# Optimization experiments

Hardware: AMD Instinct MI355X
Metric: run time of the kernel (lower is better)

Reference implementation:

```python
import jax, jax.numpy as jnp
import numpy as np

B, L, D, H, DK = 4, 256, 512, 8, 64
NEG_INF = 1.0e9


def setup_inputs() -> dict:
    key = jax.random.key(0)
    ks = jax.random.split(key, 12)
    s = 1.0 / np.sqrt(D)
    inp = {
        "q": jax.random.normal(ks[0], (B, L, D), jnp.float32),
        "k": jax.random.normal(ks[1], (B, L, D), jnp.float32),
        "v": jax.random.normal(ks[2], (B, L, D), jnp.float32),
        "mask": jnp.ones((B, L, L), jnp.int32),
        "Wq": jax.random.normal(ks[3], (D, D), jnp.float32) * s,
        "bq": jnp.zeros((D,), jnp.float32),
        "Wk": jax.random.normal(ks[4], (D, D), jnp.float32) * s,
        "bk": jnp.zeros((D,), jnp.float32),
        "Wv": jax.random.normal(ks[5], (D, D), jnp.float32) * s,
        "bv": jnp.zeros((D,), jnp.float32),
        "vp": jax.random.normal(ks[6], (1, H, 1, 1, DK), jnp.float32) * 0.1,
        "W0": jax.random.normal(ks[7], (D, D), jnp.float32) * s,
        "b0": jnp.zeros((D,), jnp.float32),
    }
    return inp


def reference(q, k, v, mask, Wq, bq, Wk, bk, Wv, bv, vp, W0, b0):
    # project and split heads: (B, L, D) -> (B, H, L, DK)
    qh = (q @ Wq + bq).reshape(B, L, H, DK).transpose(0, 2, 1, 3)
    kh = (k @ Wk + bk).reshape(B, L, H, DK).transpose(0, 2, 1, 3)
    vh = (v @ Wv + bv).reshape(B, L, H, DK).transpose(0, 2, 1, 3)
    # additive (Bahdanau) scoring: (B, H, Lq, Lk, DK) intermediate
    energy = jnp.tanh(qh[:, :, :, None, :] + kh[:, :, None, :, :])
    scores = jnp.sum(vp * energy, axis=-1)  # (B, H, Lq, Lk)
    scores = jnp.where(mask[:, None] == 0, -NEG_INF, scores)
    attn = jax.nn.softmax(scores, axis=-1)
    out = jnp.matmul(attn, vh)  # (B, H, Lq, DK)
    out = out.transpose(0, 2, 1, 3).reshape(B, L, D)
    return out @ W0 + b0
```

## Files before the change

### kernel.cpp

```cpp
#include <hip/hip_runtime.h>

#define LSEQ 256
#define DMODEL 512
#define NHEAD 8
#define DKH 64
#define BATCH 4

#define TWO_LOG2E 2.885390081777927f

using short8 = __attribute__((ext_vector_type(8))) short;
using f32x4  = __attribute__((ext_vector_type(4))) float;

__device__ __forceinline__ void split4(const float* f, ushort4& h, ushort4& l) {
  unsigned short hh[4], ll[4];
#pragma unroll
  for (int j = 0; j < 4; ++j) {
    unsigned int u = __float_as_uint(f[j]);
    hh[j] = (unsigned short)(u >> 16);
    float hf = __uint_as_float(u & 0xFFFF0000u);
    ll[j] = (unsigned short)(__float_as_uint(f[j] - hf) >> 16);
  }
  h = make_ushort4(hh[0], hh[1], hh[2], hh[3]);
  l = make_ushort4(ll[0], ll[1], ll[2], ll[3]);
}

__device__ __forceinline__ void split8(float4 f0, float4 f1, short8& h, short8& l) {
  float f[8] = {f0.x, f0.y, f0.z, f0.w, f1.x, f1.y, f1.z, f1.w};
#pragma unroll
  for (int j = 0; j < 8; ++j) {
    unsigned int u = __float_as_uint(f[j]);
    h[j] = (short)(u >> 16);
    float hf = __uint_as_float(u & 0xFFFF0000u);
    l[j] = (short)(__float_as_uint(f[j] - hf) >> 16);
  }
}

__global__ __launch_bounds__(256) void prep_w_kernel(
    const float* __restrict__ Wq, const float* __restrict__ Wk,
    const float* __restrict__ Wv, const float* __restrict__ W0,
    unsigned short* __restrict__ whi, unsigned short* __restrict__ wlo)
{
  const int tid = threadIdx.x;
  const int g = blockIdx.z;
  const float* W = (g == 0) ? Wq : (g == 1) ? Wk : (g == 2) ? Wv : W0;
  const float scale = (g < 2) ? TWO_LOG2E : 1.0f;
  const int k0 = blockIdx.x * 32, n0 = blockIdx.y * 32;
  __shared__ float tile[32][36];
  {
    const int r = tid >> 3, c = (tid & 7) << 2;
    float4 f = *(const float4*)&W[(k0 + r) * DMODEL + n0 + c];
    tile[r][c + 0] = f.x * scale;
    tile[r][c + 1] = f.y * scale;
    tile[r][c + 2] = f.z * scale;
    tile[r][c + 3] = f.w * scale;
  }
  __syncthreads();
  const int n = tid >> 3, kk = (tid & 7) << 2;
  float x[4];
#pragma unroll
  for (int j = 0; j < 4; ++j) x[j] = tile[kk + j][n];
  ushort4 h4, l4;
  split4(x, h4, l4);
  const int base = (g * DMODEL + n0 + n) * DMODEL + k0 + kk;
  *(ushort4*)&whi[base] = h4;
  *(ushort4*)&wlo[base] = l4;
}

__device__ __forceinline__ void gemm_fp32A(
    const float* __restrict__ X,
    const unsigned short* __restrict__ wh, const unsigned short* __restrict__ wl,
    const float* __restrict__ bias, float bscale,
    float* __restrict__ out, int mode, int bx, int by)
{
  __shared__ short8 lds[2][4][512];
  const int tid = threadIdx.x;
  const int lane = tid & 63, w = tid >> 6;
  const int bm0 = bx * 64, bn0 = by * 64;

  const int r0 = tid >> 3, c0 = tid & 7, g0 = c0 ^ (r0 & 7);
  const int r1 = r0 + 32,  g1 = c0 ^ (r1 & 7);
  const size_t aoff0 = (size_t)(bm0 + r0) * DMODEL + g0 * 8;
  const size_t aoff1 = (size_t)(bm0 + r1) * DMODEL + g1 * 8;
  const size_t boff0 = (size_t)(bn0 + r0) * DMODEL + g0 * 8;
  const size_t boff1 = (size_t)(bn0 + r1) * DMODEL + g1 * 8;

  const int mrb = (w >> 1) << 5, ncb = (w & 1) << 5;
  const int l15 = lane & 15, lh = lane >> 4, l7 = lane & 7;

  float4 af00, af01, af10, af11;
  short8 b0h, b0l, b1h, b1l;

#define LOADS(K)                                                  \
  { af00 = *(const float4*)(X + aoff0 + (K));                     \
    af01 = *(const float4*)(X + aoff0 + (K) + 4);                 \
    af10 = *(const float4*)(X + aoff1 + (K));                     \
    af11 = *(const float4*)(X + aoff1 + (K) + 4);                 \
    b0h = *(const short8*)(wh + boff0 + (K));                     \
    b0l = *(const short8*)(wl + boff0 + (K));                     \
    b1h = *(const short8*)(wh + boff1 + (K));                     \
    b1l = *(const short8*)(wl + boff1 + (K)); }
#define WRITES(BUF)                                               \
  { short8 h_, l_;                                                \
    split8(af00, af01, h_, l_);                                   \
    lds[BUF][0][tid] = h_; lds[BUF][1][tid] = l_;                 \
    split8(af10, af11, h_, l_);                                   \
    lds[BUF][0][tid + 256] = h_; lds[BUF][1][tid + 256] = l_;     \
    lds[BUF][2][tid] = b0h; lds[BUF][3][tid] = b0l;               \
    lds[BUF][2][tid + 256] = b1h; lds[BUF][3][tid + 256] = b1l; }

  f32x4 acc[2][2] = {};
  LOADS(0);
  WRITES(0);
  __syncthreads();

  int cur = 0;
  for (int t = 0; t < 8; ++t) {
    if (t < 7) LOADS((t + 1) * 64);
#pragma unroll
    for (int s = 0; s < 2; ++s) {
      const int chb = (s << 2) + lh;
      const int ra0 = (mrb + l15) * 8 + (chb ^ l7);
      const int ra1 = (mrb + 16 + l15) * 8 + (chb ^ l7);
      const int rb0 = (ncb + l15) * 8 + (chb ^ l7);
      const int rb1 = (ncb + 16 + l15) * 8 + (chb ^ l7);
      short8 a0h = lds[cur][0][ra0], a0l = lds[cur][1][ra0];
      short8 a1h = lds[cur][0][ra1], a1l = lds[cur][1][ra1];
      short8 w0h = lds[cur][2][rb0], w0l = lds[cur][3][rb0];
      short8 w1h = lds[cur][2][rb1], w1l = lds[cur][3][rb1];
#define MFMA_(A, B, C) C = __builtin_amdgcn_mfma_f32_16x16x32_bf16(A, B, C, 0, 0, 0)
      MFMA_(a0h, w0h, acc[0][0]); MFMA_(a0h, w0l, acc[0][0]); MFMA_(a0l, w0h, acc[0][0]);
      MFMA_(a0h, w1h, acc[0][1]); MFMA_(a0h, w1l, acc[0][1]); MFMA_(a0l, w1h, acc[0][1]);
      MFMA_(a1h, w0h, acc[1][0]); MFMA_(a1h, w0l, acc[1][0]); MFMA_(a1l, w0h, acc[1][0]);
      MFMA_(a1h, w1h, acc[1][1]); MFMA_(a1h, w1l, acc[1][1]); MFMA_(a1l, w1h, acc[1][1]);
#undef MFMA_
    }
    if (t < 7) WRITES(cur ^ 1);
    __syncthreads();
    cur ^= 1;
  }
#undef LOADS
#undef WRITES

  const int bm = bm0 + mrb, bn = bn0 + ncb;
#pragma unroll
  for (int mi = 0; mi < 2; ++mi)
#pragma unroll
    for (int ni = 0; ni < 2; ++ni) {
      const int C = bn + ni * 16 + l15;
      const float bv = bscale * bias[C];
#pragma unroll
      for (int e = 0; e < 4; ++e) {
        const int R = bm + mi * 16 + (lh << 2) + e;
        const float val = acc[mi][ni][e] + bv;
        if (mode == 0) {
          out[R * DMODEL + C] = val;
        } else {
          const int b = R >> 8, l = R & (LSEQ - 1);
          const int hh = C >> 6, dk = C & 63;
          if (mode == 1) out[((b * NHEAD + hh) * LSEQ + l) * DKH + dk] = val;
          else           out[((b * NHEAD + hh) * DKH + dk) * LSEQ + l] = val;
        }
      }
    }
}

__global__ __launch_bounds__(256) void proj_mfma_kernel(
    const float* __restrict__ q, const float* __restrict__ k, const float* __restrict__ v,
    const unsigned short* __restrict__ whi, const unsigned short* __restrict__ wlo,
    const float* __restrict__ bq, const float* __restrict__ bk, const float* __restrict__ bv,
    float* __restrict__ qh, float* __restrict__ kT, float* __restrict__ vh)
{
  int lin = blockIdx.x + 16 * blockIdx.y + 128 * blockIdx.z;
  lin = (lin & 7) * 48 + (lin >> 3);
  const int bx = lin & 15, by = (lin >> 4) & 7, g = lin >> 7;
  const unsigned short* wh = whi + (size_t)g * DMODEL * DMODEL;
  const unsigned short* wl = wlo + (size_t)g * DMODEL * DMODEL;
  if (g == 0)      gemm_fp32A(q, wh, wl, bq, TWO_LOG2E, qh, 1, bx, by);
  else if (g == 1) gemm_fp32A(k, wh, wl, bk, TWO_LOG2E, kT, 2, bx, by);
  else             gemm_fp32A(v, wh, wl, bv, 1.0f, vh, 1, bx, by);
}

__global__ __launch_bounds__(256) void outproj_mfma_kernel(
    const float* __restrict__ ao,
    const unsigned short* __restrict__ whi, const unsigned short* __restrict__ wlo,
    const float* __restrict__ b0, float* __restrict__ out)
{
  int lin = blockIdx.x + 16 * blockIdx.y;
  lin = (lin & 7) * 16 + (lin >> 3);
  const int bx = lin & 15, by = lin >> 4;
  gemm_fp32A(ao, whi + (size_t)3 * DMODEL * DMODEL,
             wlo + (size_t)3 * DMODEL * DMODEL, b0, 1.0f, out, 0, bx, by);
}

__global__ __launch_bounds__(1024, 4) void attn_kernel(
    const float* __restrict__ qh,
    const float* __restrict__ kT,
    const float* __restrict__ vh,
    const int* __restrict__ mask,
    const float* __restrict__ vp,
    float* __restrict__ ao)
{
  __shared__ float ksh[DKH][LSEQ];
  __shared__ float vsh[LSEQ][DKH];
  __shared__ float qsh[32][DKH];
  __shared__ float psh[16][LSEQ];
  __shared__ float vpsh[DKH];

  const int bh = blockIdx.x;
  const int b = bh >> 3, h = bh & 7;
  const int i0 = blockIdx.y * 32;
  const int tid = threadIdx.x;
  const int lane = tid & 63, w = tid >> 6;

  const float* kbase = kT + (size_t)bh * DKH * LSEQ;
  for (int t = tid; t < DKH * LSEQ / 4; t += 1024) {
    const int d = t >> 6, j4 = (t & 63) << 2;
    *(float4*)&ksh[d][j4] = *(const float4*)&kbase[d * LSEQ + j4];
  }
  const float* vbase = vh + (size_t)bh * LSEQ * DKH;
  for (int t = tid; t < LSEQ * DKH / 4; t += 1024) {
    const int j = t >> 4, d4 = (t & 15) << 2;
    *(float4*)&vsh[j][d4] = *(const float4*)&vbase[j * DKH + d4];
  }
  if (tid < 512) {
    const float* qbase = qh + ((size_t)bh * LSEQ + i0) * DKH;
    const int r = tid >> 4, d4 = (tid & 15) << 2;
    *(float4*)&qsh[r][d4] = *(const float4*)&qbase[r * DKH + d4];
  }
  if (tid < DKH) vpsh[tid] = vp[h * DKH + tid];
  __syncthreads();

  float tj[2][4] = {};
#pragma unroll 2
  for (int g = 0; g < 16; ++g) {
    float kv[16];
#pragma unroll
    for (int t = 0; t < 4; ++t)
#pragma unroll
      for (int c = 0; c < 4; ++c)
        kv[t * 4 + c] = ksh[(g << 2) + t][(c << 6) + lane];
    float vpv[4];
    *(float4*)vpv = *(const float4*)&vpsh[g << 2];
#pragma unroll
    for (int r = 0; r < 2; ++r) {
      float q_[4];
      *(float4*)q_ = *(const float4*)&qsh[(w << 1) + r][g << 2];
#pragma unroll
      for (int t = 0; t < 4; ++t)
#pragma unroll
        for (int c = 0; c < 4; ++c) {
          const float x = q_[t] + kv[t * 4 + c];
          const float e = __builtin_amdgcn_exp2f(x);
          tj[r][c] = fmaf(vpv[t], __builtin_amdgcn_rcpf(e + 1.f), tj[r][c]);
        }
    }
  }

  const int cg = lane >> 4, qq = lane & 15;
#pragma unroll
  for (int r = 0; r < 2; ++r) {
    const int i = i0 + (w << 1) + r;
    const int* mrow = mask + ((size_t)b * LSEQ + i) * LSEQ;
    float t4[4];
#pragma unroll
    for (int c = 0; c < 4; ++c) {
      const int mv = mrow[(c << 6) + lane];
      t4[c] = mv ? tj[r][c] : 1.0e9f;
    }
    float m = fminf(fminf(t4[0], t4[1]), fminf(t4[2], t4[3]));
#pragma unroll
    for (int off = 32; off; off >>= 1) m = fminf(m, __shfl_xor(m, off));
    const float m2 = m * TWO_LOG2E;
    float p[4];
    float sum = 0.f;
#pragma unroll
    for (int c = 0; c < 4; ++c) {
      p[c] = __builtin_amdgcn_exp2f(fmaf(t4[c], -TWO_LOG2E, m2));
      sum += p[c];
    }
#pragma unroll
    for (int off = 32; off; off >>= 1) sum += __shfl_xor(sum, off);
    const float rs = __builtin_amdgcn_rcpf(sum);
#pragma unroll
    for (int c = 0; c < 4; ++c) psh[w][(c << 6) + lane] = p[c];

    float o[4] = {0.f, 0.f, 0.f, 0.f};
#pragma unroll 4
    for (int jg = 0; jg < 16; ++jg) {
      float pv[4];
      *(float4*)pv = *(const float4*)&psh[w][(cg << 6) + (jg << 2)];
#pragma unroll
      for (int t = 0; t < 4; ++t) {
        float v_[4];
        *(float4*)v_ = *(const float4*)&vsh[(cg << 6) + (jg << 2) + t][qq << 2];
#pragma unroll
        for (int u = 0; u < 4; ++u) o[u] = fmaf(pv[t], v_[u], o[u]);
      }
    }
#pragma unroll
    for (int off = 16; off <= 32; off <<= 1) {
#pragma unroll
      for (int u = 0; u < 4; ++u) o[u] += __shfl_xor(o[u], off);
    }
    if (lane < 16) {
      float ov[4];
#pragma unroll
      for (int u = 0; u < 4; ++u) ov[u] = o[u] * rs;
      *(float4*)&ao[((size_t)b * LSEQ + i) * DMODEL + h * DKH + (qq << 2)] =
          *(float4*)ov;
    }
  }
}

extern "C" void kernel_launch(void* const* d_in, const int* in_sizes, int n_in,
                              void* d_out, int out_size, void* d_ws, size_t ws_size,
                              hipStream_t stream) {
  const float* q   = (const float*)d_in[0];
  const float* k   = (const float*)d_in[1];
  const float* v   = (const float*)d_in[2];
  const int*  mask = (const int*)d_in[3];
  const float* Wq  = (const float*)d_in[4];
  const float* bq  = (const float*)d_in[5];
  const float* Wk  = (const float*)d_in[6];
  const float* bk  = (const float*)d_in[7];
  const float* Wv  = (const float*)d_in[8];
  const float* bv  = (const float*)d_in[9];
  const float* vp  = (const float*)d_in[10];
  const float* W0  = (const float*)d_in[11];
  const float* b0  = (const float*)d_in[12];
  float* outp = (float*)d_out;

  char* wsb = (char*)d_ws;
  unsigned short* whi = (unsigned short*)(wsb);
  unsigned short* wlo = (unsigned short*)(wsb + (2u << 20));
  float* qh = (float*)(wsb + (4u << 20));
  float* kT = (float*)(wsb + (6u << 20));
  float* vh = (float*)(wsb + (8u << 20));
  float* ao = (float*)(wsb + (10u << 20));

  prep_w_kernel<<<dim3(16, 16, 4), 256, 0, stream>>>(Wq, Wk, Wv, W0, whi, wlo);
  proj_mfma_kernel<<<dim3(16, 8, 3), 256, 0, stream>>>(q, k, v, whi, wlo,
                                                       bq, bk, bv, qh, kT, vh);
  attn_kernel<<<dim3(32, 8), 1024, 0, stream>>>(qh, kT, vh, mask, vp, ao);
  outproj_mfma_kernel<<<dim3(16, 8), 256, 0, stream>>>(ao, whi, wlo, b0, outp);
}
```

Baseline: 139.7 us.

## Store K row-major with swizzled LDS, emit bf16 hi/lo attention output

The K projection is now written in the same row-major per-head layout as Q and V instead of transposed. The attention kernel stages it into LDS with an XOR swizzle and reads four dk values per key with one float4 load, rather than sixteen scalar loads per step. The attention kernel also splits its output into bf16 hi/lo halves, so the output projection can use a GEMM that reads pre-split A operands and skips the fp32 conversion in its inner loop. The trade-off is an extra 16-bit store stream from attention and more per-lane vector loads in the scoring loop, where bank conflicts could appear.

```diff
diff --git a/kernel.cpp b/kernel.cpp
--- a/kernel.cpp
+++ b/kernel.cpp
@@ -157,9 +157,93 @@
         } else {
           const int b = R >> 8, l = R & (LSEQ - 1);
           const int hh = C >> 6, dk = C & 63;
-          if (mode == 1) out[((b * NHEAD + hh) * LSEQ + l) * DKH + dk] = val;
-          else           out[((b * NHEAD + hh) * DKH + dk) * LSEQ + l] = val;
+          out[((b * NHEAD + hh) * LSEQ + l) * DKH + dk] = val;
         }
+      }
+    }
+}
+
+__device__ __forceinline__ void gemm_splitA(
+    const unsigned short* __restrict__ xh, const unsigned short* __restrict__ xl,
+    const unsigned short* __restrict__ wh, const unsigned short* __restrict__ wl,
+    const float* __restrict__ bias,
+    float* __restrict__ out, int bx, int by)
+{
+  __shared__ short8 lds[2][4][512];
+  const int tid = threadIdx.x;
+  const int lane = tid & 63, w = tid >> 6;
+  const int bm0 = bx * 64, bn0 = by * 64;
+
+  const int r0 = tid >> 3, c0 = tid & 7, g0 = c0 ^ (r0 & 7);
+  const int r1 = r0 + 32,  g1 = c0 ^ (r1 & 7);
+  const size_t aoff0 = (size_t)(bm0 + r0) * DMODEL + g0 * 8;
+  const size_t aoff1 = (size_t)(bm0 + r1) * DMODEL + g1 * 8;
+  const size_t boff0 = (size_t)(bn0 + r0) * DMODEL + g0 * 8;
+  const size_t boff1 = (size_t)(bn0 + r1) * DMODEL + g1 * 8;
+
+  const int mrb = (w >> 1) << 5, ncb = (w & 1) << 5;
+  const int l15 = lane & 15, lh = lane >> 4, l7 = lane & 7;
+
+  short8 st[8];
+#define LOADS(K)                                        \
+  { st[0] = *(const short8*)(xh + aoff0 + (K));         \
+    st[1] = *(const short8*)(xh + aoff1 + (K));         \
+    st[2] = *(const short8*)(xl + aoff0 + (K));         \
+    st[3] = *(const short8*)(xl + aoff1 + (K));         \
+    st[4] = *(const short8*)(wh + boff0 + (K));         \
+    st[5] = *(const short8*)(wh + boff1 + (K));         \
+    st[6] = *(const short8*)(wl + boff0 + (K));         \
+    st[7] = *(const short8*)(wl + boff1 + (K)); }
+#define WRITES(BUF)                                              \
+  { lds[BUF][0][tid] = st[0]; lds[BUF][0][tid + 256] = st[1];    \
+    lds[BUF][1][tid] = st[2]; lds[BUF][1][tid + 256] = st[3];    \
+    lds[BUF][2][tid] = st[4]; lds[BUF][2][tid + 256] = st[5];    \
+    lds[BUF][3][tid] = st[6]; lds[BUF][3][tid + 256] = st[7]; }
+
+  f32x4 acc[2][2] = {};
+  LOADS(0);
+  WRITES(0);
+  __syncthreads();
+
+  int cur = 0;
+  for (int t = 0; t < 8; ++t) {
+    if (t < 7) LOADS((t + 1) * 64);
+#pragma unroll
+    for (int s = 0; s < 2; ++s) {
+      const int chb = (s << 2) + lh;
+      const int ra0 = (mrb + l15) * 8 + (chb ^ l7);
+      const int ra1 = (mrb + 16 + l15) * 8 + (chb ^ l7);
+      const int rb0 = (ncb + l15) * 8 + (chb ^ l7);
+      const int rb1 = (ncb + 16 + l15) * 8 + (chb ^ l7);
+      short8 a0h = lds[cur][0][ra0], a0l = lds[cur][1][ra0];
+      short8 a1h = lds[cur][0][ra1], a1l = lds[cur][1][ra1];
+      short8 w0h = lds[cur][2][rb0], w0l = lds[cur][3][rb0];
+      short8 w1h = lds[cur][2][rb1], w1l = lds[cur][3][rb1];
+#define MFMA_(A, B, C) C = __builtin_amdgcn_mfma_f32_16x16x32_bf16(A, B, C, 0, 0, 0)
+      MFMA_(a0h, w0h, acc[0][0]); MFMA_(a0h, w0l, acc[0][0]); MFMA_(a0l, w0h, acc[0][0]);
+      MFMA_(a0h, w1h, acc[0][1]); MFMA_(a0h, w1l, acc[0][1]); MFMA_(a0l, w1h, acc[0][1]);
+      MFMA_(a1h, w0h, acc[1][0]); MFMA_(a1h, w0l, acc[1][0]); MFMA_(a1l, w0h, acc[1][0]);
+      MFMA_(a1h, w1h, acc[1][1]); MFMA_(a1h, w1l, acc[1][1]); MFMA_(a1l, w1h, acc[1][1]);
+#undef MFMA_
+    }
+    if (t < 7) WRITES(cur ^ 1);
+    __syncthreads();
+    cur ^= 1;
+  }
+#undef LOADS
+#undef WRITES
+
+  const int bm = bm0 + mrb, bn = bn0 + ncb;
+#pragma unroll
+  for (int mi = 0; mi < 2; ++mi)
+#pragma unroll
+    for (int ni = 0; ni < 2; ++ni) {
+      const int C = bn + ni * 16 + l15;
+      const float bv = bias[C];
+#pragma unroll
+      for (int e = 0; e < 4; ++e) {
+        const int R = bm + mi * 16 + (lh << 2) + e;
+        out[R * DMODEL + C] = acc[mi][ni][e] + bv;
       }
     }
 }
@@ -168,7 +252,7 @@
     const float* __restrict__ q, const float* __restrict__ k, const float* __restrict__ v,
     const unsigned short* __restrict__ whi, const unsigned short* __restrict__ wlo,
     const float* __restrict__ bq, const float* __restrict__ bk, const float* __restrict__ bv,
-    float* __restrict__ qh, float* __restrict__ kT, float* __restrict__ vh)
+    float* __restrict__ qh, float* __restrict__ kh, float* __restrict__ vh)
 {
   int lin = blockIdx.x + 16 * blockIdx.y + 128 * blockIdx.z;
   lin = (lin & 7) * 48 + (lin >> 3);
@@ -176,31 +260,32 @@
   const unsigned short* wh = whi + (size_t)g * DMODEL * DMODEL;
   const unsigned short* wl = wlo + (size_t)g * DMODEL * DMODEL;
   if (g == 0)      gemm_fp32A(q, wh, wl, bq, TWO_LOG2E, qh, 1, bx, by);
-  else if (g == 1) gemm_fp32A(k, wh, wl, bk, TWO_LOG2E, kT, 2, bx, by);
+  else if (g == 1) gemm_fp32A(k, wh, wl, bk, TWO_LOG2E, kh, 1, bx, by);
   else             gemm_fp32A(v, wh, wl, bv, 1.0f, vh, 1, bx, by);
 }
 
 __global__ __launch_bounds__(256) void outproj_mfma_kernel(
-    const float* __restrict__ ao,
+    const unsigned short* __restrict__ aoh, const unsigned short* __restrict__ aol,
     const unsigned short* __restrict__ whi, const unsigned short* __restrict__ wlo,
     const float* __restrict__ b0, float* __restrict__ out)
 {
   int lin = blockIdx.x + 16 * blockIdx.y;
   lin = (lin & 7) * 16 + (lin >> 3);
   const int bx = lin & 15, by = lin >> 4;
-  gemm_fp32A(ao, whi + (size_t)3 * DMODEL * DMODEL,
-             wlo + (size_t)3 * DMODEL * DMODEL, b0, 1.0f, out, 0, bx, by);
+  gemm_splitA(aoh, aol, whi + (size_t)3 * DMODEL * DMODEL,
+              wlo + (size_t)3 * DMODEL * DMODEL, b0, out, bx, by);
 }
 
 __global__ __launch_bounds__(1024, 4) void attn_kernel(
     const float* __restrict__ qh,
-    const float* __restrict__ kT,
+    const float* __restrict__ kh,
     const float* __restrict__ vh,
     const int* __restrict__ mask,
     const float* __restrict__ vp,
-    float* __restrict__ ao)
-{
-  __shared__ float ksh[DKH][LSEQ];
+    unsigned short* __restrict__ aoh,
+    unsigned short* __restrict__ aol)
+{
+  __shared__ float kshf[DKH * LSEQ];
   __shared__ float vsh[LSEQ][DKH];
   __shared__ float qsh[32][DKH];
   __shared__ float psh[16][LSEQ];
@@ -210,12 +295,13 @@
   const int b = bh >> 3, h = bh & 7;
   const int i0 = blockIdx.y * 32;
   const int tid = threadIdx.x;
-  const int lane = tid & 63, w = tid >> 6;
-
-  const float* kbase = kT + (size_t)bh * DKH * LSEQ;
-  for (int t = tid; t < DKH * LSEQ / 4; t += 1024) {
-    const int d = t >> 6, j4 = (t & 63) << 2;
-    *(float4*)&ksh[d][j4] = *(const float4*)&kbase[d * LSEQ + j4];
+  const int lane = tid & 63, wv = tid >> 6;
+
+  const float* kbase = kh + (size_t)bh * LSEQ * DKH;
+  for (int t = tid; t < LSEQ * DKH / 4; t += 1024) {
+    const int j = t >> 4, c4 = t & 15;
+    *(float4*)&kshf[(j << 6) + ((c4 ^ (j & 15)) << 2)] =
+        *(const float4*)&kbase[(j << 6) + (c4 << 2)];
   }
   const float* vbase = vh + (size_t)bh * LSEQ * DKH;
   for (int t = tid; t < LSEQ * DKH / 4; t += 1024) {
@@ -233,33 +319,31 @@
   float tj[2][4] = {};
 #pragma unroll 2
   for (int g = 0; g < 16; ++g) {
-    float kv[16];
-#pragma unroll
-    for (int t = 0; t < 4; ++t)
-#pragma unroll
-      for (int c = 0; c < 4; ++c)
-        kv[t * 4 + c] = ksh[(g << 2) + t][(c << 6) + lane];
-    float vpv[4];
+    float vpv[4], q0[4], q1[4];
     *(float4*)vpv = *(const float4*)&vpsh[g << 2];
-#pragma unroll
-    for (int r = 0; r < 2; ++r) {
-      float q_[4];
-      *(float4*)q_ = *(const float4*)&qsh[(w << 1) + r][g << 2];
-#pragma unroll
-      for (int t = 0; t < 4; ++t)
-#pragma unroll
-        for (int c = 0; c < 4; ++c) {
-          const float x = q_[t] + kv[t * 4 + c];
-          const float e = __builtin_amdgcn_exp2f(x);
-          tj[r][c] = fmaf(vpv[t], __builtin_amdgcn_rcpf(e + 1.f), tj[r][c]);
-        }
+    *(float4*)q0 = *(const float4*)&qsh[(wv << 1) + 0][g << 2];
+    *(float4*)q1 = *(const float4*)&qsh[(wv << 1) + 1][g << 2];
+#pragma unroll
+    for (int c = 0; c < 4; ++c) {
+      const int j = (c << 6) + lane;
+      float kv[4];
+      *(float4*)kv = *(const float4*)&kshf[(j << 6) + ((g ^ (j & 15)) << 2)];
+#pragma unroll
+      for (int t = 0; t < 4; ++t) {
+        const float x0 = q0[t] + kv[t];
+        const float e0 = __builtin_amdgcn_exp2f(x0);
+        tj[0][c] = fmaf(vpv[t], __builtin_amdgcn_rcpf(e0 + 1.f), tj[0][c]);
+        const float x1 = q1[t] + kv[t];
+        const float e1 = __builtin_amdgcn_exp2f(x1);
+        tj[1][c] = fmaf(vpv[t], __builtin_amdgcn_rcpf(e1 + 1.f), tj[1][c]);
+      }
     }
   }
 
   const int cg = lane >> 4, qq = lane & 15;
 #pragma unroll
   for (int r = 0; r < 2; ++r) {
-    const int i = i0 + (w << 1) + r;
+    const int i = i0 + (wv << 1) + r;
     const int* mrow = mask + ((size_t)b * LSEQ + i) * LSEQ;
     float t4[4];
 #pragma unroll
@@ -282,13 +366,13 @@
     for (int off = 32; off; off >>= 1) sum += __shfl_xor(sum, off);
     const float rs = __builtin_amdgcn_rcpf(sum);
 #pragma unroll
-    for (int c = 0; c < 4; ++c) psh[w][(c << 6) + lane] = p[c];
+    for (int c = 0; c < 4; ++c) psh[wv][(c << 6) + lane] = p[c];
 
     float o[4] = {0.f, 0.f, 0.f, 0.f};
 #pragma unroll 4
     for (int jg = 0; jg < 16; ++jg) {
       float pv[4];
-      *(float4*)pv = *(const float4*)&psh[w][(cg << 6) + (jg << 2)];
+      *(float4*)pv = *(const float4*)&psh[wv][(cg << 6) + (jg << 2)];
 #pragma unroll
       for (int t = 0; t < 4; ++t) {
         float v_[4];
@@ -306,8 +390,11 @@
       float ov[4];
 #pragma unroll
       for (int u = 0; u < 4; ++u) ov[u] = o[u] * rs;
-      *(float4*)&ao[((size_t)b * LSEQ + i) * DMODEL + h * DKH + (qq << 2)] =
-          *(float4*)ov;
+      ushort4 h4, l4;
+      split4(ov, h4, l4);
+      const int base = ((size_t)b * LSEQ + i) * DMODEL + h * DKH + (qq << 2);
+      *(ushort4*)&aoh[base] = h4;
+      *(ushort4*)&aol[base] = l4;
     }
   }
 }
@@ -334,13 +421,14 @@
   unsigned short* whi = (unsigned short*)(wsb);
   unsigned short* wlo = (unsigned short*)(wsb + (2u << 20));
   float* qh = (float*)(wsb + (4u << 20));
-  float* kT = (float*)(wsb + (6u << 20));
+  float* kh = (float*)(wsb + (6u << 20));
   float* vh = (float*)(wsb + (8u << 20));
-  float* ao = (float*)(wsb + (10u << 20));
+  unsigned short* aoh = (unsigned short*)(wsb + (10u << 20));
+  unsigned short* aol = (unsigned short*)(wsb + (11u << 20));
 
   prep_w_kernel<<<dim3(16, 16, 4), 256, 0, stream>>>(Wq, Wk, Wv, W0, whi, wlo);
   proj_mfma_kernel<<<dim3(16, 8, 3), 256, 0, stream>>>(q, k, v, whi, wlo,
-                                                       bq, bk, bv, qh, kT, vh);
-  attn_kernel<<<dim3(32, 8), 1024, 0, stream>>>(qh, kT, vh, mask, vp, ao);
-  outproj_mfma_kernel<<<dim3(16, 8), 256, 0, stream>>>(ao, whi, wlo, b0, outp);
-}
+                                                       bq, bk, bv, qh, kh, vh);
+  attn_kernel<<<dim3(32, 8), 1024, 0, stream>>>(qh, kh, vh, mask, vp, aoh, aol);
+  outproj_mfma_kernel<<<dim3(16, 8), 256, 0, stream>>>(aoh, aol, whi, wlo, b0, outp);
+}
```

Result: no change. 138.2 us (-1.1%).
